# Optimization experiments

Hardware: AMD Instinct MI355X
Metric: run time of the kernel (lower is better)

Reference implementation:

```python
import jax, jax.numpy as jnp
import numpy as np
from jax import lax

T, B, E = 4096, 8, 512


def setup_inputs() -> dict:
    key = jax.random.key(0)
    k1, k2, k3 = jax.random.split(key, 3)
    x = jax.random.normal(k1, (T, B, E), dtype=jnp.float32)
    raw_pos_beta = jax.random.normal(k2, (E,), dtype=jnp.float32)
    raw_neg_beta = jax.random.normal(k3, (E,), dtype=jnp.float32)
    return {"x": x, "raw_pos_beta": raw_pos_beta, "raw_neg_beta": raw_neg_beta}


def reference(x, raw_pos_beta, raw_neg_beta):
    # pos/neg split EMA. The torch module computes out[t] = sum_{s<=t} beta^(t-s) u[s]
    # via a length-T depthwise conv; that is exactly the linear recurrence
    # mem[t] = beta * mem[t-1] + u[t], which we run as an O(T) scan.
    pos_beta = jax.nn.sigmoid(raw_pos_beta)  # [E]
    neg_beta = jax.nn.sigmoid(raw_neg_beta)  # [E]
    x_pos = jnp.where(x >= 0, x, 0.0) * (1.0 - pos_beta)  # [T,B,E]
    x_neg = jnp.where(x <= 0, x, 0.0) * (1.0 - neg_beta)  # [T,B,E]
    u = jnp.stack([x_pos, x_neg], axis=-1)                # [T,B,E,2]
    beta = jnp.stack([pos_beta, neg_beta], axis=-1)       # [E,2]

    def step(carry, u_t):
        new = beta * carry + u_t  # [B,E,2]
        return new, new

    init = jnp.zeros(u.shape[1:], dtype=x.dtype)
    _, mem2 = lax.scan(step, init, u)  # [T,B,E,2]
    return mem2[..., 0] + mem2[..., 1]  # [T,B,E]
```

## Files before the change

kernel.cpp:

```cpp
#include <hip/hip_runtime.h>


#define T_DIM 4096
#define B_DIM 8
#define E_DIM 512
#define CHUNK_L 32
#define NCHUNK (T_DIM / CHUNK_L)
#define BE (B_DIM * E_DIM)

__device__ __forceinline__ float sigmoidf_(float x) { return 1.0f / (1.0f + __expf(-x)); }

__global__ __launch_bounds__(256) void k_agg(
        const float* __restrict__ x,
        const float* __restrict__ rp,
        const float* __restrict__ rn,
        float* __restrict__ agg) {
    const int gtid = blockIdx.x * 256 + threadIdx.x;
    const int q = gtid & 1023;
    const int c = gtid >> 10;
    const int e = (q & 127) * 4;
    const int b = q >> 7;
    const int col = b * E_DIM + e;

    float4 rp4 = *(const float4*)(rp + e);
    float4 rn4 = *(const float4*)(rn + e);
    float bp[4] = {sigmoidf_(rp4.x), sigmoidf_(rp4.y), sigmoidf_(rp4.z), sigmoidf_(rp4.w)};
    float bn[4] = {sigmoidf_(rn4.x), sigmoidf_(rn4.y), sigmoidf_(rn4.z), sigmoidf_(rn4.w)};

    float fp[4] = {0.f, 0.f, 0.f, 0.f};
    float fn[4] = {0.f, 0.f, 0.f, 0.f};
    const int xbase = c * CHUNK_L * BE + col;
    #pragma unroll
    for (int k = 0; k < CHUNK_L; k++) {
        float4 xv = *(const float4*)(x + xbase + k * BE);
        float f[4] = {xv.x, xv.y, xv.z, xv.w};
        #pragma unroll
        for (int j = 0; j < 4; j++) {
            fp[j] = bp[j] * fp[j] + fmaxf(f[j], 0.f) * (1.0f - bp[j]);
            fn[j] = bn[j] * fn[j] + fminf(f[j], 0.f) * (1.0f - bn[j]);
        }
    }
    *(float4*)(agg + (size_t)(c * 2 + 0) * BE + col) = make_float4(fp[0], fp[1], fp[2], fp[3]);
    *(float4*)(agg + (size_t)(c * 2 + 1) * BE + col) = make_float4(fn[0], fn[1], fn[2], fn[3]);
}

__global__ __launch_bounds__(256) void ParallelDLIEMA_17789754541002_kernel(
        const float* __restrict__ x,
        const float* __restrict__ rp,
        const float* __restrict__ rn,
        const float* __restrict__ agg,
        float* __restrict__ out) {
    const int gtid = blockIdx.x * 256 + threadIdx.x;
    const int q = gtid & 1023;
    const int c = gtid >> 10;
    const int e = (q & 127) * 4;
    const int b = q >> 7;
    const int col = b * E_DIM + e;

    float4 rp4 = *(const float4*)(rp + e);
    float4 rn4 = *(const float4*)(rn + e);
    float bp[4] = {sigmoidf_(rp4.x), sigmoidf_(rp4.y), sigmoidf_(rp4.z), sigmoidf_(rp4.w)};
    float bn[4] = {sigmoidf_(rn4.x), sigmoidf_(rn4.y), sigmoidf_(rn4.z), sigmoidf_(rn4.w)};

    float Ap[4], An[4];
    #pragma unroll
    for (int j = 0; j < 4; j++) {
        float t = bp[j] * bp[j]; t *= t; t *= t; t *= t; t *= t; Ap[j] = t;
        float u = bn[j] * bn[j]; u *= u; u *= u; u *= u; u *= u; An[j] = u;
    }

    float sp[4] = {0.f, 0.f, 0.f, 0.f};
    float sn[4] = {0.f, 0.f, 0.f, 0.f};
    #pragma unroll 4
    for (int j = 0; j < c; ++j) {
        float4 ap = *(const float4*)(agg + (size_t)(j * 2 + 0) * BE + col);
        float4 an = *(const float4*)(agg + (size_t)(j * 2 + 1) * BE + col);
        sp[0] = Ap[0] * sp[0] + ap.x;  sn[0] = An[0] * sn[0] + an.x;
        sp[1] = Ap[1] * sp[1] + ap.y;  sn[1] = An[1] * sn[1] + an.y;
        sp[2] = Ap[2] * sp[2] + ap.z;  sn[2] = An[2] * sn[2] + an.z;
        sp[3] = Ap[3] * sp[3] + ap.w;  sn[3] = An[3] * sn[3] + an.w;
    }

    const int xbase = c * CHUNK_L * BE + col;
    #pragma unroll
    for (int k = 0; k < CHUNK_L; k++) {
        float4 xv = *(const float4*)(x + xbase + k * BE);
        float f[4] = {xv.x, xv.y, xv.z, xv.w};
        float o[4];
        #pragma unroll
        for (int j = 0; j < 4; j++) {
            sp[j] = bp[j] * sp[j] + fmaxf(f[j], 0.f) * (1.0f - bp[j]);
            sn[j] = bn[j] * sn[j] + fminf(f[j], 0.f) * (1.0f - bn[j]);
            o[j] = sp[j] + sn[j];
        }
        *(float4*)(out + xbase + k * BE) = make_float4(o[0], o[1], o[2], o[3]);
    }
}


#define FB_CHUNK_L 16
#define FB_NCHUNK (T_DIM / FB_CHUNK_L)

__global__ __launch_bounds__(256) void k1_local(
        const float* __restrict__ x, const float* __restrict__ rp,
        const float* __restrict__ rn, float* __restrict__ out) {
    int gtid = blockIdx.x * 256 + threadIdx.x;
    int e4 = gtid & 127; int b = (gtid >> 7) & 7; int c = gtid >> 10; int e = e4 * 4;
    float4 rp4 = *(const float4*)(rp + e);
    float4 rn4 = *(const float4*)(rn + e);
    float bp[4] = {sigmoidf_(rp4.x), sigmoidf_(rp4.y), sigmoidf_(rp4.z), sigmoidf_(rp4.w)};
    float bn[4] = {sigmoidf_(rn4.x), sigmoidf_(rn4.y), sigmoidf_(rn4.z), sigmoidf_(rn4.w)};
    float fp4[4] = {0.f,0.f,0.f,0.f}, fn4[4] = {0.f,0.f,0.f,0.f};
    int base = c * FB_CHUNK_L * BE + b * E_DIM + e;
    #pragma unroll
    for (int k = 0; k < FB_CHUNK_L; k++) {
        float4 xv = *(const float4*)(x + base + k * BE);
        float f[4] = {xv.x, xv.y, xv.z, xv.w};
        #pragma unroll
        for (int j = 0; j < 4; j++) {
            fp4[j] = bp[j] * fp4[j] + fmaxf(f[j], 0.f) * (1.0f - bp[j]);
            fn4[j] = bn[j] * fn4[j] + fminf(f[j], 0.f) * (1.0f - bn[j]);
        }
    }
    *(float4*)(out + base + 0 * BE) = make_float4(fp4[0], fp4[1], fp4[2], fp4[3]);
    *(float4*)(out + base + 1 * BE) = make_float4(fn4[0], fn4[1], fn4[2], fn4[3]);
}

__global__ __launch_bounds__(256) void k_carry(const float* __restrict__ rp,
                                               const float* __restrict__ rn,
                                               float* __restrict__ out) {
    int gtid = blockIdx.x * 256 + threadIdx.x;
    int e = gtid & 511; int b = (gtid >> 9) & 7; int s = gtid >> 12;
    float beta = sigmoidf_(s ? rn[e] : rp[e]);
    float bl = beta * beta; bl = bl * bl; bl = bl * bl; bl = bl * bl;
    float* p = out + s * BE + b * E_DIM + e;
    float carry = 0.f;
    for (int g = 0; g < FB_NCHUNK / 16; g++) {
        float fv[16];
        #pragma unroll
        for (int u = 0; u < 16; u++) fv[u] = p[(g * 16 + u) * (FB_CHUNK_L * BE)];
        #pragma unroll
        for (int u = 0; u < 16; u++) {
            p[(g * 16 + u) * (FB_CHUNK_L * BE)] = carry;
            carry = bl * carry + fv[u];
        }
    }
}

__global__ __launch_bounds__(256) void k_out(const float* __restrict__ x,
                                             const float* __restrict__ rp,
                                             const float* __restrict__ rn,
                                             float* __restrict__ out) {
    int gtid = blockIdx.x * 256 + threadIdx.x;
    int e4 = gtid & 127; int b = (gtid >> 7) & 7; int c = gtid >> 10; int e = e4 * 4;
    float4 rp4 = *(const float4*)(rp + e);
    float4 rn4 = *(const float4*)(rn + e);
    float bp[4] = {sigmoidf_(rp4.x), sigmoidf_(rp4.y), sigmoidf_(rp4.z), sigmoidf_(rp4.w)};
    float bn[4] = {sigmoidf_(rn4.x), sigmoidf_(rn4.y), sigmoidf_(rn4.z), sigmoidf_(rn4.w)};
    int base = c * FB_CHUNK_L * BE + b * E_DIM + e;
    float4 cp = *(const float4*)(out + base + 0 * BE);
    float4 cn = *(const float4*)(out + base + 1 * BE);
    float lp[4] = {cp.x, cp.y, cp.z, cp.w};
    float ln[4] = {cn.x, cn.y, cn.z, cn.w};
    #pragma unroll
    for (int k = 0; k < FB_CHUNK_L; k++) {
        float4 xv = *(const float4*)(x + base + k * BE);
        float f[4] = {xv.x, xv.y, xv.z, xv.w};
        float o[4];
        #pragma unroll
        for (int j = 0; j < 4; j++) {
            lp[j] = bp[j] * lp[j] + fmaxf(f[j], 0.f) * (1.0f - bp[j]);
            ln[j] = bn[j] * ln[j] + fminf(f[j], 0.f) * (1.0f - bn[j]);
            o[j] = lp[j] + ln[j];
        }
        *(float4*)(out + base + k * BE) = make_float4(o[0], o[1], o[2], o[3]);
    }
}

extern "C" void kernel_launch(void* const* d_in, const int* in_sizes, int n_in,
                              void* d_out, int out_size, void* d_ws, size_t ws_size,
                              hipStream_t stream) {
    const float* x  = (const float*)d_in[0];
    const float* rp = (const float*)d_in[1];
    const float* rn = (const float*)d_in[2];
    float* out = (float*)d_out;

    const size_t need = (size_t)2 * NCHUNK * BE * sizeof(float);
    if (d_ws != nullptr && ws_size >= need) {
        float* agg = (float*)d_ws;
        k_agg<<<512, 256, 0, stream>>>(x, rp, rn, agg);
        ParallelDLIEMA_17789754541002_kernel<<<512, 256, 0, stream>>>(x, rp, rn, agg, out);
    } else {
        k1_local<<<1024, 256, 0, stream>>>(x, rp, rn, out);
        k_carry<<<32, 256, 0, stream>>>(rp, rn, out);
        k_out<<<1024, 256, 0, stream>>>(x, rp, rn, out);
    }
}
```

Measured before the change: 129.7 us.

## Compute chunk carries with in-block scan instead of per-thread serial prefix

The first kernel now computes the per-chunk local aggregates for a 16-column slice across all 128 chunks in one block, stores them in shared memory, and runs a blocked parallel (Hillis-Steele) scan over chunks to produce each chunk's incoming carry. The output kernel then loads a single carry per chunk instead of looping over all previous chunk aggregates, which removed an O(NCHUNK) serial reload from global memory per thread. The cost is more barriers and a 256-block grid of 512 threads with sizable shared memory in the first kernel, which may reduce occupancy and latency hiding there.

```diff
diff --git a/kernel.cpp b/kernel.cpp
--- a/kernel.cpp
+++ b/kernel.cpp
@@ -9,46 +9,94 @@
 #define BE (B_DIM * E_DIM)
 
 __device__ __forceinline__ float sigmoidf_(float x) { return 1.0f / (1.0f + __expf(-x)); }
-
-__global__ __launch_bounds__(256) void k_agg(
+__device__ __forceinline__ float pow32_(float b) { float t = b * b; t *= t; t *= t; t *= t; t *= t; return t; }
+
+__global__ __launch_bounds__(512) void k_carr(
         const float* __restrict__ x,
         const float* __restrict__ rp,
         const float* __restrict__ rn,
-        float* __restrict__ agg) {
-    const int gtid = blockIdx.x * 256 + threadIdx.x;
-    const int q = gtid & 1023;
-    const int c = gtid >> 10;
-    const int e = (q & 127) * 4;
-    const int b = q >> 7;
-    const int col = b * E_DIM + e;
-
-    float4 rp4 = *(const float4*)(rp + e);
-    float4 rn4 = *(const float4*)(rn + e);
-    float bp[4] = {sigmoidf_(rp4.x), sigmoidf_(rp4.y), sigmoidf_(rp4.z), sigmoidf_(rp4.w)};
-    float bn[4] = {sigmoidf_(rn4.x), sigmoidf_(rn4.y), sigmoidf_(rn4.z), sigmoidf_(rn4.w)};
-
-    float fp[4] = {0.f, 0.f, 0.f, 0.f};
-    float fn[4] = {0.f, 0.f, 0.f, 0.f};
-    const int xbase = c * CHUNK_L * BE + col;
-    #pragma unroll
-    for (int k = 0; k < CHUNK_L; k++) {
-        float4 xv = *(const float4*)(x + xbase + k * BE);
-        float f[4] = {xv.x, xv.y, xv.z, xv.w};
-        #pragma unroll
-        for (int j = 0; j < 4; j++) {
-            fp[j] = bp[j] * fp[j] + fmaxf(f[j], 0.f) * (1.0f - bp[j]);
-            fn[j] = bn[j] * fn[j] + fminf(f[j], 0.f) * (1.0f - bn[j]);
-        }
-    }
-    *(float4*)(agg + (size_t)(c * 2 + 0) * BE + col) = make_float4(fp[0], fp[1], fp[2], fp[3]);
-    *(float4*)(agg + (size_t)(c * 2 + 1) * BE + col) = make_float4(fn[0], fn[1], fn[2], fn[3]);
+        float* __restrict__ carr) {
+    __shared__ float Fs[NCHUNK * 33];
+    __shared__ float sA[16 * 32];
+    __shared__ float sB[16 * 32];
+
+    const int e0g = blockIdx.x * 16;
+    const int tid = threadIdx.x;
+
+    {
+        const int c   = tid >> 2;
+        const int qg  = tid & 3;
+        const int cg0 = e0g + qg * 4;
+        const int eb  = cg0 & 511;
+        float4 rp4 = *(const float4*)(rp + eb);
+        float4 rn4 = *(const float4*)(rn + eb);
+        float bp[4] = {sigmoidf_(rp4.x), sigmoidf_(rp4.y), sigmoidf_(rp4.z), sigmoidf_(rp4.w)};
+        float bn[4] = {sigmoidf_(rn4.x), sigmoidf_(rn4.y), sigmoidf_(rn4.z), sigmoidf_(rn4.w)};
+        float fp[4] = {0.f, 0.f, 0.f, 0.f};
+        float fn[4] = {0.f, 0.f, 0.f, 0.f};
+        const size_t xb = (size_t)c * CHUNK_L * BE + cg0;
+        #pragma unroll
+        for (int k = 0; k < CHUNK_L; k++) {
+            float4 xv = *(const float4*)(x + xb + (size_t)k * BE);
+            float f[4] = {xv.x, xv.y, xv.z, xv.w};
+            #pragma unroll
+            for (int j = 0; j < 4; j++) {
+                fp[j] = bp[j] * fp[j] + fmaxf(f[j], 0.f) * (1.0f - bp[j]);
+                fn[j] = bn[j] * fn[j] + fminf(f[j], 0.f) * (1.0f - bn[j]);
+            }
+        }
+        const int sc0 = qg * 4;
+        #pragma unroll
+        for (int j = 0; j < 4; j++) {
+            Fs[c * 33 + sc0 + j]      = fp[j];
+            Fs[c * 33 + 16 + sc0 + j] = fn[j];
+        }
+    }
+    __syncthreads();
+
+    const int sc   = tid & 31;
+    const int cg   = tid >> 5;
+    const int colg = e0g + (sc & 15);
+    const int s    = sc >> 4;
+    const float beta = sigmoidf_((s ? rn : rp)[colg & 511]);
+    const float A = pow32_(beta);
+
+    float B8 = 0.f;
+    #pragma unroll
+    for (int u = 0; u < 8; u++) B8 = A * B8 + Fs[(cg * 8 + u) * 33 + sc];
+    float A8; { float t = A * A; t *= t; A8 = t * t; }
+
+    float curA = A8, curB = B8;
+    #pragma unroll
+    for (int d = 1; d < 16; d <<= 1) {
+        sA[cg * 32 + sc] = curA;
+        sB[cg * 32 + sc] = curB;
+        __syncthreads();
+        if (cg >= d) {
+            float pA = sA[(cg - d) * 32 + sc];
+            float pB = sB[(cg - d) * 32 + sc];
+            curB = curA * pB + curB;
+            curA = curA * pA;
+        }
+        __syncthreads();
+    }
+    sB[cg * 32 + sc] = curB;
+    __syncthreads();
+    float E = (cg == 0) ? 0.f : sB[(cg - 1) * 32 + sc];
+
+    #pragma unroll
+    for (int u = 0; u < 8; u++) {
+        const int c = cg * 8 + u;
+        carr[(size_t)(c * 2 + s) * BE + colg] = E;
+        E = A * E + Fs[c * 33 + sc];
+    }
 }
 
 __global__ __launch_bounds__(256) void ParallelDLIEMA_17789754541002_kernel(
         const float* __restrict__ x,
         const float* __restrict__ rp,
         const float* __restrict__ rn,
-        const float* __restrict__ agg,
+        const float* __restrict__ carr,
         float* __restrict__ out) {
     const int gtid = blockIdx.x * 256 + threadIdx.x;
     const int q = gtid & 1023;
@@ -62,29 +110,15 @@
     float bp[4] = {sigmoidf_(rp4.x), sigmoidf_(rp4.y), sigmoidf_(rp4.z), sigmoidf_(rp4.w)};
     float bn[4] = {sigmoidf_(rn4.x), sigmoidf_(rn4.y), sigmoidf_(rn4.z), sigmoidf_(rn4.w)};
 
-    float Ap[4], An[4];
-    #pragma unroll
-    for (int j = 0; j < 4; j++) {
-        float t = bp[j] * bp[j]; t *= t; t *= t; t *= t; t *= t; Ap[j] = t;
-        float u = bn[j] * bn[j]; u *= u; u *= u; u *= u; u *= u; An[j] = u;
-    }
-
-    float sp[4] = {0.f, 0.f, 0.f, 0.f};
-    float sn[4] = {0.f, 0.f, 0.f, 0.f};
-    #pragma unroll 4
-    for (int j = 0; j < c; ++j) {
-        float4 ap = *(const float4*)(agg + (size_t)(j * 2 + 0) * BE + col);
-        float4 an = *(const float4*)(agg + (size_t)(j * 2 + 1) * BE + col);
-        sp[0] = Ap[0] * sp[0] + ap.x;  sn[0] = An[0] * sn[0] + an.x;
-        sp[1] = Ap[1] * sp[1] + ap.y;  sn[1] = An[1] * sn[1] + an.y;
-        sp[2] = Ap[2] * sp[2] + ap.z;  sn[2] = An[2] * sn[2] + an.z;
-        sp[3] = Ap[3] * sp[3] + ap.w;  sn[3] = An[3] * sn[3] + an.w;
-    }
-
-    const int xbase = c * CHUNK_L * BE + col;
+    float4 cp = *(const float4*)(carr + (size_t)(c * 2 + 0) * BE + col);
+    float4 cn = *(const float4*)(carr + (size_t)(c * 2 + 1) * BE + col);
+    float sp[4] = {cp.x, cp.y, cp.z, cp.w};
+    float sn[4] = {cn.x, cn.y, cn.z, cn.w};
+
+    const size_t xbase = (size_t)c * CHUNK_L * BE + col;
     #pragma unroll
     for (int k = 0; k < CHUNK_L; k++) {
-        float4 xv = *(const float4*)(x + xbase + k * BE);
+        float4 xv = *(const float4*)(x + xbase + (size_t)k * BE);
         float f[4] = {xv.x, xv.y, xv.z, xv.w};
         float o[4];
         #pragma unroll
@@ -93,7 +127,7 @@
             sn[j] = bn[j] * sn[j] + fminf(f[j], 0.f) * (1.0f - bn[j]);
             o[j] = sp[j] + sn[j];
         }
-        *(float4*)(out + xbase + k * BE) = make_float4(o[0], o[1], o[2], o[3]);
+        *(float4*)(out + xbase + (size_t)k * BE) = make_float4(o[0], o[1], o[2], o[3]);
     }
 }
 
@@ -187,9 +221,9 @@
 
     const size_t need = (size_t)2 * NCHUNK * BE * sizeof(float);
     if (d_ws != nullptr && ws_size >= need) {
-        float* agg = (float*)d_ws;
-        k_agg<<<512, 256, 0, stream>>>(x, rp, rn, agg);
-        ParallelDLIEMA_17789754541002_kernel<<<512, 256, 0, stream>>>(x, rp, rn, agg, out);
+        float* carr = (float*)d_ws;
+        k_carr<<<256, 512, 0, stream>>>(x, rp, rn, carr);
+        ParallelDLIEMA_17789754541002_kernel<<<512, 256, 0, stream>>>(x, rp, rn, carr, out);
     } else {
         k1_local<<<1024, 256, 0, stream>>>(x, rp, rn, out);
         k_carry<<<32, 256, 0, stream>>>(rp, rn, out);
```

New measurement: 139.1 us. 1.07x slower.
